# Optimization experiments

Measured on AMD Instinct MI355X. Metric: run time of the kernel, lower is better.

The kernel has to match this reference:

```python
import jax, jax.numpy as jnp
import numpy as np

HEAD_DIM = 128


def _apply_rotary(x, cos, sin):
    # x: [B, S, H, HD]; cos/sin: [S, HD//2]
    xr = x.reshape(*x.shape[:-1], -1, 2)  # interleaved pairs
    xe, xo = xr[..., 0], xr[..., 1]
    c = cos[None, :, None, :]
    s = sin[None, :, None, :]
    oe = xe * c - xo * s
    oo = xe * s + xo * c
    return jnp.stack([oe, oo], axis=-1).reshape(x.shape)


def setup_inputs() -> dict:
    key = jax.random.key(0)
    ks = jax.random.split(key, 8)
    B, S, D = 2, 1024, 4096
    KVD = 1024  # n_kv_heads * head_dim = 8 * 128
    MAXB, MAXS, KVH, HD = 2, 2048, 8, HEAD_DIM
    theta = 500000.0
    # rotary tables (real/imag of freqs_cis)
    inv = 1.0 / theta ** (np.arange(0, HD, 2)[: HD // 2].astype(np.float32) / HD)
    t = np.arange(S, dtype=np.float32)
    fr = np.outer(t, inv)
    sc = 0.02
    return {
        "x": jax.random.normal(ks[0], (B, S, D), jnp.float32),
        "wq": jax.random.normal(ks[1], (D, D), jnp.float32) * sc,
        "wk": jax.random.normal(ks[2], (D, KVD), jnp.float32) * sc,
        "wv": jax.random.normal(ks[3], (D, KVD), jnp.float32) * sc,
        "wo": jax.random.normal(ks[4], (D, D), jnp.float32) * sc,
        "freqs_cos": jnp.asarray(np.cos(fr)),
        "freqs_sin": jnp.asarray(np.sin(fr)),
        "cache_k": jnp.zeros((MAXB, MAXS, KVH, HD), jnp.float32),
        "cache_v": jnp.zeros((MAXB, MAXS, KVH, HD), jnp.float32),
        "start_pos": 0,
    }


def reference(x, wq, wk, wv, wo, freqs_cos, freqs_sin, cache_k, cache_v, start_pos):
    B, S, D = x.shape
    HD = HEAD_DIM
    H = wq.shape[1] // HD
    KVH = wk.shape[1] // HD
    n_rep = H // KVH

    xq = (x @ wq).reshape(B, S, H, HD)
    xk = (x @ wk).reshape(B, S, KVH, HD)
    xv = (x @ wv).reshape(B, S, KVH, HD)

    xq = _apply_rotary(xq, freqs_cos, freqs_sin)
    xk = _apply_rotary(xk, freqs_cos, freqs_sin)

    # KV-cache update (scatter at start_pos), then read back prefix
    cache_k = cache_k.at[:B, start_pos:start_pos + S].set(xk)
    cache_v = cache_v.at[:B, start_pos:start_pos + S].set(xv)
    keys = cache_k[:B, : start_pos + S]    # [B, T, KVH, HD]
    values = cache_v[:B, : start_pos + S]

    # GQA: repeat kv heads
    keys = jnp.repeat(keys, n_rep, axis=2)      # [B, T, H, HD]
    values = jnp.repeat(values, n_rep, axis=2)

    scale = 1.0 / jnp.sqrt(jnp.float32(HD))
    scores = jnp.einsum("bshd,bthd->bhst", xq, keys) * scale  # [B, H, S, T]

    # causal mask: zeros for the start_pos prefix, upper-triangular -inf after
    T = start_pos + S
    causal = jnp.triu(jnp.full((S, S), -jnp.inf, jnp.float32), k=1)
    mask = jnp.concatenate([jnp.zeros((S, start_pos), jnp.float32), causal], axis=1)  # [S, T]
    scores = scores + mask[None, None, :, :]

    probs = jax.nn.softmax(scores, axis=-1)
    out = jnp.einsum("bhst,bthd->bshd", probs, values).reshape(B, S, D)
    return out @ wo
```

## Files before the change

kernel.cpp:

```cpp
#include <hip/hip_runtime.h>
#include <stdint.h>

#define B_    2
#define S_    1024
#define D_    4096
#define KVD_  1024
#define H_    32
#define KVH_  8
#define HD_   128
#define M_    (B_ * S_)
#define N1_   (D_ + 2 * KVD_)
#define QK_SCALE_L2E (0.08838834764831845f * 1.4426950408889634f)

typedef __attribute__((ext_vector_type(8))) short bf16x8;
typedef __attribute__((ext_vector_type(4))) float f32x4;
typedef __attribute__((ext_vector_type(4))) unsigned short u16x4;
typedef __attribute__((ext_vector_type(8))) unsigned short u16x8;

__device__ inline unsigned short f2bf(float f) {
  unsigned u = __float_as_uint(f);
  u += 0x7FFFu + ((u >> 16) & 1u);
  return (unsigned short)(u >> 16);
}
__device__ inline float bf2f(unsigned short b) {
  return __uint_as_float(((unsigned)b) << 16);
}

#define ASYNC_LD16(g, l) __builtin_amdgcn_global_load_lds( \
    (const __attribute__((address_space(1))) void*)(g),    \
    (__attribute__((address_space(3))) void*)(l), 16, 0, 0)

#define MFMA16(a, b, c) __builtin_amdgcn_mfma_f32_16x16x32_bf16(a, b, c, 0, 0, 0)

#define WAIT_LGKM0() do { asm volatile("s_waitcnt lgkmcnt(0)" ::: "memory"); \
                          __builtin_amdgcn_sched_barrier(0); } while (0)
#define SCHED_PIN() __builtin_amdgcn_sched_barrier(0)
#define BAR() __builtin_amdgcn_s_barrier()

__global__ __launch_bounds__(256) void k_cvt_x(const float* __restrict__ x,
                                               unsigned short* __restrict__ xb) {
  size_t i = ((size_t)blockIdx.x * 256 + threadIdx.x) * 4;
  float4 v = *(const float4*)(x + i);
  u16x4 o;
  o[0] = f2bf(v.x); o[1] = f2bf(v.y); o[2] = f2bf(v.z); o[3] = f2bf(v.w);
  *(u16x4*)(xb + i) = o;
}

__global__ __launch_bounds__(256) void k_transpose_all(const float* __restrict__ wq,
                                                       const float* __restrict__ wk,
                                                       const float* __restrict__ wv,
                                                       const float* __restrict__ wo,
                                                       unsigned short* __restrict__ w1t,
                                                       unsigned short* __restrict__ wot) {
  int bid = blockIdx.x;
  const float* in; unsigned short* out; int C, bx, by;
  if (bid < 4096)      { in = wq; out = w1t;                          C = 4096; bx = bid & 63; by = bid >> 6; }
  else if (bid < 5120) { bid -= 4096; in = wk; out = w1t + (size_t)D_ * D_;            C = 1024; bx = bid & 15; by = bid >> 4; }
  else if (bid < 6144) { bid -= 5120; in = wv; out = w1t + (size_t)(D_ + KVD_) * D_;   C = 1024; bx = bid & 15; by = bid >> 4; }
  else                 { bid -= 6144; in = wo; out = wot;                              C = 4096; bx = bid & 63; by = bid >> 6; }
  const int R = 4096;
  __shared__ unsigned short tile[64][72];
  int t = threadIdx.x;
  int c0 = bx * 64, r0 = by * 64;
#pragma unroll
  for (int j = 0; j < 4; ++j) {
    int r = (t >> 4) + 16 * j;
    int c = (t & 15) * 4;
    float4 v = *(const float4*)(in + (size_t)(r0 + r) * C + c0 + c);
    tile[r][c + 0] = f2bf(v.x); tile[r][c + 1] = f2bf(v.y);
    tile[r][c + 2] = f2bf(v.z); tile[r][c + 3] = f2bf(v.w);
  }
  __syncthreads();
#pragma unroll
  for (int j = 0; j < 2; ++j) {
    int cc = (t >> 3) + 32 * j;
    int r = (t & 7) * 8;
    u16x8 o;
#pragma unroll
    for (int i = 0; i < 8; ++i) o[i] = tile[r + i][cc];
    *(u16x8*)(out + (size_t)(c0 + cc) * R + r0 + r) = o;
  }
}

__global__ __launch_bounds__(512, 4) void k_gemm_g1(const unsigned short* __restrict__ A,
                                                    const unsigned short* __restrict__ Bt,
                                                    unsigned short* __restrict__ C,
                                                    const float* __restrict__ fc,
                                                    const float* __restrict__ fs) {
  __shared__ unsigned short L[40960];
  const int tid = threadIdx.x, lane = tid & 63, w = tid >> 6;
  const int l15 = lane & 15, l4 = lane >> 4;
  const int wm = w >> 2, wn = w & 3;
  const int brow = blockIdx.y * 128, bcol = blockIdx.x * 192;
  const unsigned short* gA = A + (size_t)brow * 4096;
  const unsigned short* gB = Bt + (size_t)bcol * 4096;
  const int scol = ((lane & 7) ^ (lane >> 3)) * 8;

#define G1_ST_A(bb, kt, r) ASYNC_LD16( \
    gA + (size_t)((r) * 64 + w * 8 + (lane >> 3)) * 4096 + (kt) * 64 + scol, \
    L + (bb) + ((r) * 64 + w * 8) * 64)
#define G1_ST_B(bb, kt, r) ASYNC_LD16( \
    gB + (size_t)((r) * 64 + w * 8 + (lane >> 3)) * 4096 + (kt) * 64 + scol, \
    L + (bb) + 8192 + ((r) * 64 + w * 8) * 64)

  f32x4 acc[4][3] = {};
  bf16x8 bfr[3][2], af[2][2];

  G1_ST_A(0, 0, 0); G1_ST_A(0, 0, 1);
  G1_ST_B(0, 0, 0); G1_ST_B(0, 0, 1); G1_ST_B(0, 0, 2);
  G1_ST_B(20480, 1, 0); G1_ST_B(20480, 1, 1); G1_ST_B(20480, 1, 2);
  asm volatile("s_waitcnt vmcnt(3)" ::: "memory");
  SCHED_PIN();
  BAR();

  for (int t = 0; t < 64; ++t) {
    const int cb = (t & 1) * 20480, nb = cb ^ 20480;

#pragma unroll
    for (int nf = 0; nf < 3; ++nf)
#pragma unroll
      for (int ks = 0; ks < 2; ++ks)
        bfr[nf][ks] = *(const bf16x8*)(L + cb + 8192 +
            (wn * 48 + nf * 16 + l15) * 64 + ((ks * 4 + l4) ^ (l15 & 7)) * 8);
#pragma unroll
    for (int i = 0; i < 2; ++i)
#pragma unroll
      for (int ks = 0; ks < 2; ++ks)
        af[i][ks] = *(const bf16x8*)(L + cb +
            (wm * 64 + i * 16 + l15) * 64 + ((ks * 4 + l4) ^ (l15 & 7)) * 8);
    if (t + 1 < 64) { G1_ST_A(nb, t + 1, 0); G1_ST_A(nb, t + 1, 1); }
    SCHED_PIN(); BAR(); WAIT_LGKM0();
    __builtin_amdgcn_s_setprio(1);
#pragma unroll
    for (int i = 0; i < 2; ++i)
#pragma unroll
      for (int nf = 0; nf < 3; ++nf)
#pragma unroll
        for (int ks = 0; ks < 2; ++ks)
          acc[i][nf] = MFMA16(af[i][ks], bfr[nf][ks], acc[i][nf]);
    __builtin_amdgcn_s_setprio(0);
    BAR();

#pragma unroll
    for (int i = 0; i < 2; ++i)
#pragma unroll
      for (int ks = 0; ks < 2; ++ks)
        af[i][ks] = *(const bf16x8*)(L + cb +
            (wm * 64 + (2 + i) * 16 + l15) * 64 + ((ks * 4 + l4) ^ (l15 & 7)) * 8);
    if (t + 2 < 64) { G1_ST_B(cb, t + 2, 0); G1_ST_B(cb, t + 2, 1); G1_ST_B(cb, t + 2, 2); }
    SCHED_PIN(); BAR(); WAIT_LGKM0();
    __builtin_amdgcn_s_setprio(1);
#pragma unroll
    for (int i = 0; i < 2; ++i)
#pragma unroll
      for (int nf = 0; nf < 3; ++nf)
#pragma unroll
        for (int ks = 0; ks < 2; ++ks)
          acc[2 + i][nf] = MFMA16(af[i][ks], bfr[nf][ks], acc[2 + i][nf]);
    __builtin_amdgcn_s_setprio(0);
    if (t + 2 < 64) { asm volatile("s_waitcnt vmcnt(3)" ::: "memory"); }
    else            { asm volatile("s_waitcnt vmcnt(0)" ::: "memory"); }
    SCHED_PIN();
    BAR();
  }
#undef G1_ST_A
#undef G1_ST_B

#pragma unroll
  for (int mf = 0; mf < 4; ++mf)
#pragma unroll
    for (int nf = 0; nf < 3; ++nf)
#pragma unroll
      for (int q = 0; q < 4; ++q) {
        int row = brow + wm * 64 + mf * 16 + l4 * 4 + q;
        int col = bcol + wn * 48 + nf * 16 + l15;
        float v = acc[mf][nf][q];
        float p = __shfl_xor(v, 1);
        float r;
        if (col < D_ + KVD_) {
          int i = (col & 127) >> 1, s = row & (S_ - 1);
          float c = fc[s * 64 + i], sn = fs[s * 64 + i];
          bool ev = (col & 1) == 0;
          float xe = ev ? v : p, xo = ev ? p : v;
          r = ev ? (xe * c - xo * sn) : (xe * sn + xo * c);
          if (col < D_) r *= QK_SCALE_L2E;
        } else r = v;
        C[(size_t)row * N1_ + col] = f2bf(r);
      }
}

__global__ __launch_bounds__(512, 2) void k_gemm_g2(const unsigned short* __restrict__ A,
                                                    const unsigned short* __restrict__ Bt,
                                                    float* __restrict__ C) {
  __shared__ unsigned short L[2 * 24576];
  const int tid = threadIdx.x, lane = tid & 63, w = tid >> 6;
  const int l15 = lane & 15, l4 = lane >> 4;
  const int wm = w >> 2, wn = w & 3;
  const int brow = blockIdx.y * 128, bcol = blockIdx.x * 256;
  const unsigned short* gA = A + (size_t)brow * 4096;
  const unsigned short* gB = Bt + (size_t)bcol * 4096;
  const int srow = lane >> 3;
  const int scol = ((lane & 7) ^ (srow & 7)) * 8;

#define G2_ST_A(buf, kt, r0) ASYNC_LD16( \
    gA + (size_t)((r0) + w * 8 + srow) * 4096 + (kt) * 64 + scol, \
    L + (buf) * 24576 + ((r0) + w * 8) * 64)
#define G2_ST_B(buf, kt, r0) ASYNC_LD16( \
    gB + (size_t)((r0) + w * 8 + srow) * 4096 + (kt) * 64 + scol, \
    L + (buf) * 24576 + 8192 + ((r0) + w * 8) * 64)
#define G2_ST_TILE(buf, kt) do { \
    G2_ST_A(buf, kt, 0); G2_ST_A(buf, kt, 64); \
    G2_ST_B(buf, kt, 0); G2_ST_B(buf, kt, 64); G2_ST_B(buf, kt, 128); G2_ST_B(buf, kt, 192); } while (0)

  const int aoff0 = (wm * 64 + l15) * 64 + ((l4 + 0) ^ (l15 & 7)) * 8;
  const int aoff1 = (wm * 64 + l15) * 64 + ((l4 + 4) ^ (l15 & 7)) * 8;
  const int boff0 = 8192 + (wn * 64 + l15) * 64 + ((l4 + 0) ^ (l15 & 7)) * 8;
  const int boff1 = 8192 + (wn * 64 + l15) * 64 + ((l4 + 4) ^ (l15 & 7)) * 8;

  f32x4 acc[4][4] = {};

  G2_ST_TILE(0, 0);
  G2_ST_TILE(1, 1);
  asm volatile("s_waitcnt vmcnt(6)" ::: "memory");
  BAR();

  for (int t = 0; t < 64; ++t) {
    const unsigned short* Lc = L + (t & 1) * 24576;
    bf16x8 af[4], bk[4];

#pragma unroll
    for (int m = 0; m < 4; ++m) af[m] = *(const bf16x8*)(Lc + aoff0 + m * 1024);
#pragma unroll
    for (int n = 0; n < 4; ++n) bk[n] = *(const bf16x8*)(Lc + boff0 + n * 1024);
    SCHED_PIN(); BAR(); WAIT_LGKM0();
    __builtin_amdgcn_s_setprio(1);
#pragma unroll
    for (int m = 0; m < 4; ++m)
#pragma unroll
      for (int n = 0; n < 4; ++n) acc[m][n] = MFMA16(af[m], bk[n], acc[m][n]);
    __builtin_amdgcn_s_setprio(0);
    BAR();

#pragma unroll
    for (int m = 0; m < 4; ++m) af[m] = *(const bf16x8*)(Lc + aoff1 + m * 1024);
#pragma unroll
    for (int n = 0; n < 4; ++n) bk[n] = *(const bf16x8*)(Lc + boff1 + n * 1024);
    SCHED_PIN(); BAR(); WAIT_LGKM0();
    __builtin_amdgcn_s_setprio(1);
#pragma unroll
    for (int m = 0; m < 4; ++m)
#pragma unroll
      for (int n = 0; n < 4; ++n) acc[m][n] = MFMA16(af[m], bk[n], acc[m][n]);
    __builtin_amdgcn_s_setprio(0);
    SCHED_PIN();
    if (t + 2 < 64) {
      G2_ST_TILE(t & 1, t + 2);
      asm volatile("s_waitcnt vmcnt(6)" ::: "memory");
    } else if (t + 1 < 64) {
      asm volatile("s_waitcnt vmcnt(0)" ::: "memory");
    }
    BAR();
  }
#undef G2_ST_TILE
#undef G2_ST_A
#undef G2_ST_B

#pragma unroll
  for (int mf = 0; mf < 4; ++mf)
#pragma unroll
    for (int nf = 0; nf < 4; ++nf)
#pragma unroll
      for (int q = 0; q < 4; ++q) {
        int row = brow + wm * 64 + mf * 16 + l4 * 4 + q;
        int col = bcol + wn * 64 + nf * 16 + l15;
        C[(size_t)row * D_ + col] = acc[mf][nf][q];
      }
}

__global__ __launch_bounds__(256) void k_transpose_v(const unsigned short* __restrict__ qkv,
                                                     unsigned short* __restrict__ vt) {
  int bh = blockIdx.z;
  int d0 = blockIdx.x * 64;
  int s0 = blockIdx.y * 64;
  __shared__ unsigned short tile[64][72];
  int t = threadIdx.x;
  const unsigned short* src = qkv + (size_t)(bh >> 3) * S_ * N1_ + D_ + KVD_ + (bh & 7) * HD_;
#pragma unroll
  for (int j = 0; j < 2; ++j) {
    int s = (t >> 3) + 32 * j;
    int d = (t & 7) * 8;
    u16x8 v = *(const u16x8*)(src + (size_t)(s0 + s) * N1_ + d0 + d);
#pragma unroll
    for (int i = 0; i < 8; ++i) tile[s][d + i] = v[i];
  }
  __syncthreads();
#pragma unroll
  for (int j = 0; j < 2; ++j) {
    int d = (t >> 3) + 32 * j;
    int s = (t & 7) * 8;
    u16x8 o;
#pragma unroll
    for (int i = 0; i < 8; ++i) o[i] = tile[s + i][d];
    *(u16x8*)(vt + (size_t)(bh * HD_ + d0 + d) * S_ + s0 + s) = o;
  }
}

__global__ __launch_bounds__(256) void k_flash(const unsigned short* __restrict__ qkv,
                                               const unsigned short* __restrict__ vt,
                                               unsigned short* __restrict__ ao) {
  int f = blockIdx.x;
  int bh = f >> 3;
  int qt = (f & 256) ? (7 - (f & 7)) : (f & 7);
  int b = bh >> 5, h = bh & 31;
  int kh = h >> 2;
  int tid = threadIdx.x, lane = tid & 63, w = tid >> 6;
  int l15 = lane & 15, l4 = lane >> 4;

  __shared__ unsigned short Ks[2 * 64 * 128];
  __shared__ unsigned short Vs[2 * 128 * 64];
  __shared__ unsigned short Ps[4][32 * 64];

  int qb0 = qt * 128;
  int rwb = qb0 + w * 32;
  int NT = 2 * qt + 2;

  const unsigned short* qp = qkv + (size_t)(b * S_ + rwb) * N1_ + h * HD_;
  bf16x8 qf[2][4];
#pragma unroll
  for (int qr = 0; qr < 2; ++qr)
#pragma unroll
    for (int ks = 0; ks < 4; ++ks)
      qf[qr][ks] = *(const bf16x8*)(qp + (size_t)(qr * 16 + l15) * N1_ + ks * 32 + l4 * 8);

  f32x4 o[2][8];
#pragma unroll
  for (int qr = 0; qr < 2; ++qr)
#pragma unroll
    for (int d = 0; d < 8; ++d) o[qr][d] = (f32x4){0.f, 0.f, 0.f, 0.f};
  float lrun[2][4];
#pragma unroll
  for (int qr = 0; qr < 2; ++qr)
#pragma unroll
    for (int q = 0; q < 4; ++q) lrun[qr][q] = 0.f;

  const unsigned short* kbase = qkv + (size_t)(b * S_) * N1_ + D_ + kh * HD_;
  const unsigned short* vbase = vt + (size_t)(b * KVH_ + kh) * HD_ * S_;
  int krl = lane >> 4, kcu = lane & 15;
  int vrl = lane >> 3, vcu = lane & 7;

#define STAGE_KV(bo, itt) do {                                               \
    int kv0s = (itt) * 64;                                                   \
    _Pragma("unroll")                                                        \
    for (int j = 0; j < 4; ++j) {                                            \
      int kc = w * 4 + j;                                                    \
      int krow = kc * 4 + krl;                                               \
      int su = kcu ^ (krow & 7);                                             \
      ASYNC_LD16(kbase + (size_t)(kv0s + krow) * N1_ + su * 8,               \
                 Ks + (bo) * 8192 + kc * 512);                               \
      int vrow = kc * 8 + vrl;                                               \
      int sv = vcu ^ (vrow & 7);                                             \
      ASYNC_LD16(vbase + (size_t)vrow * S_ + kv0s + sv * 8,                  \
                 Vs + (bo) * 8192 + kc * 512);                               \
    }                                                                        \
  } while (0)

  int cur = 0;
  STAGE_KV(0, 0);

  for (int it = 0; it < NT; ++it) {
    int kv0 = it * 64;
    if (it + 1 < NT) {
      STAGE_KV(cur ^ 1, it + 1);
      asm volatile("s_waitcnt vmcnt(8)" ::: "memory");
    } else {
      asm volatile("s_waitcnt vmcnt(0)" ::: "memory");
    }
    __builtin_amdgcn_s_barrier();
    __builtin_amdgcn_sched_barrier(0);

    if (kv0 <= rwb + 31) {
      const unsigned short* Kc = Ks + cur * 8192;
      const unsigned short* Vc = Vs + cur * 8192;

      f32x4 sf[2][4] = {};
      __builtin_amdgcn_s_setprio(1);
#pragma unroll
      for (int ks = 0; ks < 4; ++ks)
#pragma unroll
        for (int n = 0; n < 4; ++n) {
          int row = n * 16 + l15;
          int u = (l4 + ks * 4) ^ (row & 7);
          bf16x8 kf = *(const bf16x8*)(Kc + row * 128 + u * 8);
          sf[0][n] = MFMA16(qf[0][ks], kf, sf[0][n]);
          sf[1][n] = MFMA16(qf[1][ks], kf, sf[1][n]);
        }
      __builtin_amdgcn_s_setprio(0);

      if (kv0 + 63 > rwb) {
#pragma unroll
        for (int qr = 0; qr < 2; ++qr)
#pragma unroll
          for (int n = 0; n < 4; ++n)
#pragma unroll
            for (int q = 0; q < 4; ++q) {
              int rq = rwb + qr * 16 + l4 * 4 + q;
              int ck = kv0 + n * 16 + l15;
              if (ck > rq) sf[qr][n][q] = -1e30f;
            }
      }

#pragma unroll
      for (int qr = 0; qr < 2; ++qr)
#pragma unroll
        for (int n = 0; n < 4; ++n)
#pragma unroll
          for (int q = 0; q < 4; ++q) {
            float p = __builtin_amdgcn_exp2f(sf[qr][n][q]);
            sf[qr][n][q] = p;
            lrun[qr][q] += p;
          }

      unsigned short* pw = Ps[w];
#pragma unroll
      for (int qr = 0; qr < 2; ++qr)
#pragma unroll
        for (int n = 0; n < 4; ++n)
#pragma unroll
          for (int q = 0; q < 4; ++q) {
            int rp = qr * 16 + l4 * 4 + q;
            int cp = n * 16 + l15;
            pw[rp * 64 + (((cp >> 3) ^ (rp & 7)) * 8) + (cp & 7)] = f2bf(sf[qr][n][q]);
          }

      __builtin_amdgcn_s_setprio(1);
#pragma unroll
      for (int kvs = 0; kvs < 2; ++kvs) {
        bf16x8 pa0 = *(const bf16x8*)(pw + (l15) * 64 + (((l4 + kvs * 4) ^ (l15 & 7)) * 8));
        bf16x8 pa1 = *(const bf16x8*)(pw + (16 + l15) * 64 + (((l4 + kvs * 4) ^ (l15 & 7)) * 8));
#pragma unroll
        for (int d = 0; d < 8; ++d) {
          int vrow = d * 16 + l15;
          int u = (l4 + kvs * 4) ^ (vrow & 7);
          bf16x8 vf = *(const bf16x8*)(Vc + vrow * 64 + u * 8);
          o[0][d] = MFMA16(pa0, vf, o[0][d]);
          o[1][d] = MFMA16(pa1, vf, o[1][d]);
        }
      }
      __builtin_amdgcn_s_setprio(0);
    }

    __builtin_amdgcn_s_barrier();
    cur ^= 1;
  }
#undef STAGE_KV

  float invl[2][4];
#pragma unroll
  for (int qr = 0; qr < 2; ++qr)
#pragma unroll
    for (int q = 0; q < 4; ++q) {
      float s = lrun[qr][q];
#pragma unroll
      for (int off = 1; off < 16; off <<= 1) s += __shfl_xor(s, off, 16);
      invl[qr][q] = 1.f / s;
    }
#pragma unroll
  for (int qr = 0; qr < 2; ++qr)
#pragma unroll
    for (int d = 0; d < 8; ++d)
#pragma unroll
      for (int q = 0; q < 4; ++q) {
        int row = b * S_ + rwb + qr * 16 + l4 * 4 + q;
        ao[(size_t)row * D_ + h * HD_ + d * 16 + l15] = f2bf(o[qr][d][q] * invl[qr][q]);
      }
}

extern "C" void kernel_launch(void* const* d_in, const int* in_sizes, int n_in,
                              void* d_out, int out_size, void* d_ws, size_t ws_size,
                              hipStream_t stream) {
  const float* x  = (const float*)d_in[0];
  const float* wq = (const float*)d_in[1];
  const float* wk = (const float*)d_in[2];
  const float* wv = (const float*)d_in[3];
  const float* wo = (const float*)d_in[4];
  const float* fc = (const float*)d_in[5];
  const float* fs = (const float*)d_in[6];
  float* out = (float*)d_out;

  char* ws = (char*)d_ws;
  unsigned short* xb  = (unsigned short*)ws; ws += (size_t)M_ * D_ * 2;
  unsigned short* w1t = (unsigned short*)ws; ws += (size_t)N1_ * D_ * 2;
  unsigned short* wot = (unsigned short*)ws; ws += (size_t)D_ * D_ * 2;
  unsigned short* qkv = (unsigned short*)ws; ws += (size_t)M_ * N1_ * 2;
  unsigned short* vtb = (unsigned short*)ws; ws += (size_t)B_ * KVH_ * HD_ * S_ * 2;
  unsigned short* ao  = (unsigned short*)ws; ws += (size_t)M_ * D_ * 2;

  k_cvt_x<<<(M_ * D_) / 1024, 256, 0, stream>>>(x, xb);
  k_transpose_all<<<10240, 256, 0, stream>>>(wq, wk, wv, wo, w1t, wot);

  k_gemm_g1<<<dim3(N1_ / 192, M_ / 128), 512, 0, stream>>>(xb, w1t, qkv, fc, fs);

  k_transpose_v<<<dim3(2, 16, 16), 256, 0, stream>>>(qkv, vtb);
  k_flash<<<dim3(512), 256, 0, stream>>>(qkv, vtb, ao);

  k_gemm_g2<<<dim3(D_ / 256, M_ / 128), 512, 0, stream>>>(ao, wot, out);
}
```

Baseline: 270.5 us.

## Halve flash attention tile sizes and swizzle GEMM block order for locality

The flash kernel now uses 64-row query tiles (16 rows per wave) and 32-key KV tiles, doubling the grid to 1024 blocks and cutting per-wave registers and shared memory so more blocks can be resident. The load-balancing pairing of query tiles is rewritten for 16 tiles per head. Both GEMMs remap their linear block index with a grouped swizzle so that blocks running at the same time share A and B tiles in cache. The trade-off is more K/V reloads per query row, smaller MFMA batches and more barriers per unit of work.

```diff
diff --git a/kernel.cpp b/kernel.cpp
--- a/kernel.cpp
+++ b/kernel.cpp
@@ -91,7 +91,9 @@
   const int tid = threadIdx.x, lane = tid & 63, w = tid >> 6;
   const int l15 = lane & 15, l4 = lane >> 4;
   const int wm = w >> 2, wn = w & 3;
-  const int brow = blockIdx.y * 128, bcol = blockIdx.x * 192;
+  int lin = blockIdx.y * 32 + blockIdx.x;
+  int swz = (lin & 7) * 64 + (lin >> 3);
+  const int brow = (swz >> 5) * 128, bcol = (swz & 31) * 192;
   const unsigned short* gA = A + (size_t)brow * 4096;
   const unsigned short* gB = Bt + (size_t)bcol * 4096;
   const int scol = ((lane & 7) ^ (lane >> 3)) * 8;
@@ -196,7 +198,9 @@
   const int tid = threadIdx.x, lane = tid & 63, w = tid >> 6;
   const int l15 = lane & 15, l4 = lane >> 4;
   const int wm = w >> 2, wn = w & 3;
-  const int brow = blockIdx.y * 128, bcol = blockIdx.x * 256;
+  int lin = blockIdx.y * 16 + blockIdx.x;
+  int swz = (lin & 7) * 32 + (lin >> 3);
+  const int brow = (swz >> 4) * 128, bcol = (swz & 15) * 256;
   const unsigned short* gA = A + (size_t)brow * 4096;
   const unsigned short* gB = Bt + (size_t)bcol * 4096;
   const int srow = lane >> 3;
@@ -305,62 +309,54 @@
   }
 }
 
-__global__ __launch_bounds__(256) void k_flash(const unsigned short* __restrict__ qkv,
-                                               const unsigned short* __restrict__ vt,
-                                               unsigned short* __restrict__ ao) {
+__global__ __launch_bounds__(256, 4) void k_flash(const unsigned short* __restrict__ qkv,
+                                                  const unsigned short* __restrict__ vt,
+                                                  unsigned short* __restrict__ ao) {
   int f = blockIdx.x;
-  int bh = f >> 3;
-  int qt = (f & 256) ? (7 - (f & 7)) : (f & 7);
+  int bh = f >> 4;
+  int i16 = f & 15;
+  int qt = (bh & 1) ? 15 - i16 : i16;
   int b = bh >> 5, h = bh & 31;
   int kh = h >> 2;
   int tid = threadIdx.x, lane = tid & 63, w = tid >> 6;
   int l15 = lane & 15, l4 = lane >> 4;
 
-  __shared__ unsigned short Ks[2 * 64 * 128];
-  __shared__ unsigned short Vs[2 * 128 * 64];
-  __shared__ unsigned short Ps[4][32 * 64];
-
-  int qb0 = qt * 128;
-  int rwb = qb0 + w * 32;
+  __shared__ unsigned short Ks[2 * 32 * 128];
+  __shared__ unsigned short Vs[2 * 128 * 32];
+  __shared__ unsigned short Ps[4][16 * 32];
+
+  int rwb = qt * 64 + w * 16;
   int NT = 2 * qt + 2;
 
   const unsigned short* qp = qkv + (size_t)(b * S_ + rwb) * N1_ + h * HD_;
-  bf16x8 qf[2][4];
-#pragma unroll
-  for (int qr = 0; qr < 2; ++qr)
-#pragma unroll
-    for (int ks = 0; ks < 4; ++ks)
-      qf[qr][ks] = *(const bf16x8*)(qp + (size_t)(qr * 16 + l15) * N1_ + ks * 32 + l4 * 8);
-
-  f32x4 o[2][8];
-#pragma unroll
-  for (int qr = 0; qr < 2; ++qr)
-#pragma unroll
-    for (int d = 0; d < 8; ++d) o[qr][d] = (f32x4){0.f, 0.f, 0.f, 0.f};
-  float lrun[2][4];
-#pragma unroll
-  for (int qr = 0; qr < 2; ++qr)
-#pragma unroll
-    for (int q = 0; q < 4; ++q) lrun[qr][q] = 0.f;
+  bf16x8 qf[4];
+#pragma unroll
+  for (int ks = 0; ks < 4; ++ks)
+    qf[ks] = *(const bf16x8*)(qp + (size_t)l15 * N1_ + ks * 32 + l4 * 8);
+
+  f32x4 o[8];
+#pragma unroll
+  for (int d = 0; d < 8; ++d) o[d] = (f32x4){0.f, 0.f, 0.f, 0.f};
+  float lrun[4] = {0.f, 0.f, 0.f, 0.f};
 
   const unsigned short* kbase = qkv + (size_t)(b * S_) * N1_ + D_ + kh * HD_;
   const unsigned short* vbase = vt + (size_t)(b * KVH_ + kh) * HD_ * S_;
   int krl = lane >> 4, kcu = lane & 15;
-  int vrl = lane >> 3, vcu = lane & 7;
+  int vrl = lane >> 2, vcu = lane & 3;
 
 #define STAGE_KV(bo, itt) do {                                               \
-    int kv0s = (itt) * 64;                                                   \
+    int kv0s = (itt) * 32;                                                   \
     _Pragma("unroll")                                                        \
-    for (int j = 0; j < 4; ++j) {                                            \
-      int kc = w * 4 + j;                                                    \
+    for (int j = 0; j < 2; ++j) {                                            \
+      int kc = w * 2 + j;                                                    \
       int krow = kc * 4 + krl;                                               \
       int su = kcu ^ (krow & 7);                                             \
       ASYNC_LD16(kbase + (size_t)(kv0s + krow) * N1_ + su * 8,               \
-                 Ks + (bo) * 8192 + kc * 512);                               \
-      int vrow = kc * 8 + vrl;                                               \
-      int sv = vcu ^ (vrow & 7);                                             \
+                 Ks + (bo) * 4096 + kc * 512);                               \
+      int vrow = kc * 16 + vrl;                                              \
+      int sv = vcu ^ (vrow & 3);                                             \
       ASYNC_LD16(vbase + (size_t)vrow * S_ + kv0s + sv * 8,                  \
-                 Vs + (bo) * 8192 + kc * 512);                               \
+                 Vs + (bo) * 4096 + kc * 512);                               \
     }                                                                        \
   } while (0)
 
@@ -368,83 +364,71 @@
   STAGE_KV(0, 0);
 
   for (int it = 0; it < NT; ++it) {
-    int kv0 = it * 64;
+    int kv0 = it * 32;
     if (it + 1 < NT) {
       STAGE_KV(cur ^ 1, it + 1);
-      asm volatile("s_waitcnt vmcnt(8)" ::: "memory");
+      asm volatile("s_waitcnt vmcnt(4)" ::: "memory");
     } else {
       asm volatile("s_waitcnt vmcnt(0)" ::: "memory");
     }
     __builtin_amdgcn_s_barrier();
     __builtin_amdgcn_sched_barrier(0);
 
-    if (kv0 <= rwb + 31) {
-      const unsigned short* Kc = Ks + cur * 8192;
-      const unsigned short* Vc = Vs + cur * 8192;
-
-      f32x4 sf[2][4] = {};
+    if (kv0 <= rwb + 15) {
+      const unsigned short* Kc = Ks + cur * 4096;
+      const unsigned short* Vc = Vs + cur * 4096;
+
+      f32x4 sf[2] = {};
       __builtin_amdgcn_s_setprio(1);
 #pragma unroll
       for (int ks = 0; ks < 4; ++ks)
 #pragma unroll
-        for (int n = 0; n < 4; ++n) {
+        for (int n = 0; n < 2; ++n) {
           int row = n * 16 + l15;
           int u = (l4 + ks * 4) ^ (row & 7);
           bf16x8 kf = *(const bf16x8*)(Kc + row * 128 + u * 8);
-          sf[0][n] = MFMA16(qf[0][ks], kf, sf[0][n]);
-          sf[1][n] = MFMA16(qf[1][ks], kf, sf[1][n]);
+          sf[n] = MFMA16(qf[ks], kf, sf[n]);
         }
       __builtin_amdgcn_s_setprio(0);
 
-      if (kv0 + 63 > rwb) {
-#pragma unroll
-        for (int qr = 0; qr < 2; ++qr)
-#pragma unroll
-          for (int n = 0; n < 4; ++n)
-#pragma unroll
-            for (int q = 0; q < 4; ++q) {
-              int rq = rwb + qr * 16 + l4 * 4 + q;
-              int ck = kv0 + n * 16 + l15;
-              if (ck > rq) sf[qr][n][q] = -1e30f;
-            }
+      if (kv0 + 31 > rwb) {
+#pragma unroll
+        for (int n = 0; n < 2; ++n)
+#pragma unroll
+          for (int q = 0; q < 4; ++q) {
+            int rq = rwb + l4 * 4 + q;
+            int ck = kv0 + n * 16 + l15;
+            if (ck > rq) sf[n][q] = -1e30f;
+          }
       }
 
 #pragma unroll
-      for (int qr = 0; qr < 2; ++qr)
-#pragma unroll
-        for (int n = 0; n < 4; ++n)
-#pragma unroll
-          for (int q = 0; q < 4; ++q) {
-            float p = __builtin_amdgcn_exp2f(sf[qr][n][q]);
-            sf[qr][n][q] = p;
-            lrun[qr][q] += p;
-          }
+      for (int n = 0; n < 2; ++n)
+#pragma unroll
+        for (int q = 0; q < 4; ++q) {
+          float p = __builtin_amdgcn_exp2f(sf[n][q]);
+          sf[n][q] = p;
+          lrun[q] += p;
+        }
 
       unsigned short* pw = Ps[w];
 #pragma unroll
-      for (int qr = 0; qr < 2; ++qr)
-#pragma unroll
-        for (int n = 0; n < 4; ++n)
-#pragma unroll
-          for (int q = 0; q < 4; ++q) {
-            int rp = qr * 16 + l4 * 4 + q;
-            int cp = n * 16 + l15;
-            pw[rp * 64 + (((cp >> 3) ^ (rp & 7)) * 8) + (cp & 7)] = f2bf(sf[qr][n][q]);
-          }
+      for (int n = 0; n < 2; ++n)
+#pragma unroll
+        for (int q = 0; q < 4; ++q) {
+          int rp = l4 * 4 + q;
+          int cp = n * 16 + l15;
+          pw[rp * 32 + (((cp >> 3) ^ (rp & 3)) * 8) + (cp & 7)] = f2bf(sf[n][q]);
+        }
 
       __builtin_amdgcn_s_setprio(1);
-#pragma unroll
-      for (int kvs = 0; kvs < 2; ++kvs) {
-        bf16x8 pa0 = *(const bf16x8*)(pw + (l15) * 64 + (((l4 + kvs * 4) ^ (l15 & 7)) * 8));
-        bf16x8 pa1 = *(const bf16x8*)(pw + (16 + l15) * 64 + (((l4 + kvs * 4) ^ (l15 & 7)) * 8));
-#pragma unroll
-        for (int d = 0; d < 8; ++d) {
-          int vrow = d * 16 + l15;
-          int u = (l4 + kvs * 4) ^ (vrow & 7);
-          bf16x8 vf = *(const bf16x8*)(Vc + vrow * 64 + u * 8);
-          o[0][d] = MFMA16(pa0, vf, o[0][d]);
-          o[1][d] = MFMA16(pa1, vf, o[1][d]);
-        }
+      bf16x8 pa = *(const bf16x8*)(pw + l15 * 32 + ((l4 ^ (l15 & 3)) * 8));
+#pragma unroll
+      for (int d = 0; d < 8; ++d) {
+        int vrow = d * 16 + l15;
+        int u = l4 ^ (vrow & 3);
+        bf16x8 vf = *(const bf16x8*)(Vc + vrow * 32 + u * 8);
+        o[d] = MFMA16(pa, vf, o[d]);
       }
       __builtin_amdgcn_s_setprio(0);
     }
@@ -454,25 +438,21 @@
   }
 #undef STAGE_KV
 
-  float invl[2][4];
-#pragma unroll
-  for (int qr = 0; qr < 2; ++qr)
+  float invl[4];
+#pragma unroll
+  for (int q = 0; q < 4; ++q) {
+    float s = lrun[q];
+#pragma unroll
+    for (int off = 1; off < 16; off <<= 1) s += __shfl_xor(s, off, 16);
+    invl[q] = 1.f / s;
+  }
+#pragma unroll
+  for (int d = 0; d < 8; ++d)
 #pragma unroll
     for (int q = 0; q < 4; ++q) {
-      float s = lrun[qr][q];
-#pragma unroll
-      for (int off = 1; off < 16; off <<= 1) s += __shfl_xor(s, off, 16);
-      invl[qr][q] = 1.f / s;
+      int row = b * S_ + rwb + l4 * 4 + q;
+      ao[(size_t)row * D_ + h * HD_ + d * 16 + l15] = f2bf(o[d][q] * invl[q]);
     }
-#pragma unroll
-  for (int qr = 0; qr < 2; ++qr)
-#pragma unroll
-    for (int d = 0; d < 8; ++d)
-#pragma unroll
-      for (int q = 0; q < 4; ++q) {
-        int row = b * S_ + rwb + qr * 16 + l4 * 4 + q;
-        ao[(size_t)row * D_ + h * HD_ + d * 16 + l15] = f2bf(o[qr][d][q] * invl[qr][q]);
-      }
 }
 
 extern "C" void kernel_launch(void* const* d_in, const int* in_sizes, int n_in,
@@ -501,7 +481,7 @@
   k_gemm_g1<<<dim3(N1_ / 192, M_ / 128), 512, 0, stream>>>(xb, w1t, qkv, fc, fs);
 
   k_transpose_v<<<dim3(2, 16, 16), 256, 0, stream>>>(qkv, vtb);
-  k_flash<<<dim3(512), 256, 0, stream>>>(qkv, vtb, ao);
+  k_flash<<<dim3(1024), 256, 0, stream>>>(qkv, vtb, ao);
 
   k_gemm_g2<<<dim3(D_ / 256, M_ / 128), 512, 0, stream>>>(ao, wot, out);
 }
```

Result: slower. 301.9 us (+11.6%).
